# Kernel tuning notes

Hardware: AMD Instinct MI355X
Metric: run time of the kernel (lower is better)

## Reference

```python
import jax, jax.numpy as jnp
import numpy as np

EPS = 1e-5  # InstanceNorm2d default eps


def mesh_conv_point(x, neighbors, W, b):
    """MeshConvPoint: gather self+neighbor features, apply 1x(K+1) conv.
    x: [B, C, N]; neighbors: [B, N, K] int; W: [Cout, C, K+1]; b: [Cout]
    returns [B, Cout, N]
    """
    # gather neighbor features per batch: [B, C, N, K]
    g = jax.vmap(lambda xb, nb: xb[:, nb])(x, neighbors)
    G = jnp.concatenate([x[..., None], g], axis=-1)  # [B, C, N, K+1]
    return jnp.einsum('bcnk,ock->bon', G, W) + b[None, :, None]


def instance_norm(x):
    # InstanceNorm2d (affine=False) on [B, C, N, 1] == normalize over N per (b,c)
    mu = jnp.mean(x, axis=2, keepdims=True)
    var = jnp.var(x, axis=2, keepdims=True)
    return (x - mu) * jax.lax.rsqrt(var + EPS)


def setup_inputs() -> dict:
    key = jax.random.key(0)
    ks = jax.random.split(key, 10)
    B, Cin, Cout, N, K = 2, 256, 128, 30000, 6
    from_up = jax.random.normal(ks[0], (B, Cin, N), dtype=jnp.float32)
    from_down = jax.random.normal(ks[1], (B, Cout, N), dtype=jnp.float32)
    neighbors = jax.random.randint(ks[2], (B, N, K), 0, N)
    s = 0.05
    W_up = jax.random.normal(ks[3], (Cout, Cin, K + 1), dtype=jnp.float32) * s
    b_up = jnp.zeros((Cout,), dtype=jnp.float32)
    W_1 = jax.random.normal(ks[4], (Cout, 2 * Cout, K + 1), dtype=jnp.float32) * s
    b_1 = jnp.zeros((Cout,), dtype=jnp.float32)
    W_2 = jax.random.normal(ks[5], (Cout, Cout, K + 1), dtype=jnp.float32) * s
    b_2 = jnp.zeros((Cout,), dtype=jnp.float32)
    return {"from_up": from_up, "from_down": from_down, "neighbors": neighbors,
            "W_up": W_up, "b_up": b_up, "W_1": W_1, "b_1": b_1,
            "W_2": W_2, "b_2": b_2}


def reference(from_up, from_down, neighbors, W_up, b_up, W_1, b_1, W_2, b_2):
    # up_conv + squeeze(3)
    x1 = mesh_conv_point(from_up, neighbors, W_up, b_up)          # [B, Cout, N]
    # transfer_data: concat skip features along channels
    x1 = jnp.concatenate([x1, from_down], axis=1)                 # [B, 2*Cout, N]
    x1 = mesh_conv_point(x1, neighbors, W_1, b_1)                 # [B, Cout, N]
    x1 = instance_norm(x1)                                        # bn[0]
    # one conv2 block (blocks=1): conv + instance norm + residual
    x2 = mesh_conv_point(x1, neighbors, W_2, b_2)
    x2 = instance_norm(x2)                                        # bn[1]
    x2 = x2 + x1                                                  # residual
    return x2                                                     # [B, Cout, N]
```

## Files before the change

kernel.cpp:

```cpp
#include <hip/hip_runtime.h>

typedef __attribute__((ext_vector_type(8))) short short8;
typedef __attribute__((ext_vector_type(4))) float f32x4;

static __device__ __forceinline__ float bf2f(unsigned short u) {
    unsigned int x = ((unsigned int)u) << 16;
    union { unsigned int i; float f; } c; c.i = x; return c.f;
}
static __device__ __forceinline__ unsigned short f2bf(float f) {
    union { float f; unsigned int i; } c; c.f = f;
    unsigned int x = c.i;
    unsigned int r = (x + 0x7FFFu + ((x >> 16) & 1u)) >> 16;
    return (unsigned short)r;
}
static __device__ __forceinline__ void glds16(const char* g, char* l) {
    __builtin_amdgcn_global_load_lds(
        (const __attribute__((address_space(1))) unsigned int*)g,
        (__attribute__((address_space(3))) unsigned int*)l, 16, 0, 0);
}

__global__ void prepack_w2(const float* __restrict__ Wa, const float* __restrict__ Wb,
                           unsigned short* __restrict__ Wpa, unsigned short* __restrict__ Wpb,
                           int S) {
    int tid = blockIdx.x * blockDim.x + threadIdx.x;
    if (tid >= 2 * S * 512) return;
    const float* W = (tid < S * 512) ? Wa : Wb;
    unsigned short* Wp = (tid < S * 512) ? Wpa : Wpb;
    int rem = (tid < S * 512) ? tid : tid - S * 512;
    const int Cin = 256;
    int lane = rem & 63;
    int f = (rem >> 6) & 7;
    int s = rem >> 9;
    int o = f * 16 + (lane & 15);
    int kbase = s * 32 + 8 * (lane >> 4);
    unsigned short* dst = Wp + (size_t)rem * 8;
#pragma unroll
    for (int j = 0; j < 8; ++j) {
        int kk = kbase + j;
        int t = kk / Cin;
        int c = kk - t * Cin;
        dst[j] = f2bf(W[((size_t)o * Cin + c) * 7 + t]);
    }
}

__global__ void prepack_scaled_fold(const float* __restrict__ W, const float2* __restrict__ stats,
                                    unsigned short* __restrict__ Wp, const float* __restrict__ b2,
                                    float* __restrict__ b2out, int S, int nPre) {
    if ((int)blockIdx.x < nPre) {
        int tid = blockIdx.x * 256 + threadIdx.x;
        const int Cin = 128;
        int b = tid / (S * 512);
        int rem = tid - b * S * 512;
        int lane = rem & 63;
        int f = (rem >> 6) & 7;
        int s = rem >> 9;
        int o = f * 16 + (lane & 15);
        int kbase = s * 32 + 8 * (lane >> 4);
        unsigned short* dst = Wp + (size_t)tid * 8;
#pragma unroll
        for (int j = 0; j < 8; ++j) {
            int kk = kbase + j;
            int t = kk / Cin;
            int c = kk - t * Cin;
            float scale = stats[b * 128 + c].y;
            dst[j] = f2bf(W[((size_t)o * Cin + c) * 7 + t] * scale);
        }
    } else {
        int b = threadIdx.x >> 7, o = threadIdx.x & 127;
        float sum = 0.f;
        for (int c = 0; c < 128; ++c) {
            float2 st = stats[b * 128 + c];
            float sm = st.x * st.y;
            float ws = 0.f;
#pragma unroll
            for (int t = 0; t < 7; ++t) ws += W[((size_t)o * 128 + c) * 7 + t];
            sum += ws * sm;
        }
        b2out[b * 128 + o] = b2[o] - sum;
    }
}

__global__ void transpose_cast2(const float* __restrict__ up, const float* __restrict__ down,
                                unsigned short* __restrict__ upT, unsigned short* __restrict__ catT,
                                int N) {
    __shared__ __align__(16) unsigned short T[64 * 72];
    int b = blockIdx.z;
    int y = blockIdx.y;
    const float* in;  unsigned short* outp;  int c0, coff, C;
    if (y < 4) { in = up;   outp = upT;  c0 = y * 64;       coff = 0;   C = 256; }
    else       { in = down; outp = catT; c0 = (y - 4) * 64; coff = 128; C = 128; }
    int n0 = blockIdx.x * 64;
    const float* inb = in + (size_t)b * C * N;
    unsigned short* outb = outp + (size_t)b * N * 256;
    int tid = threadIdx.x;

    int nq = tid & 15, c_l = tid >> 4;
    bool nv = (n0 + nq * 4) < N;
    float4 v[4];
#pragma unroll
    for (int ci = 0; ci < 4; ++ci) {
        v[ci] = make_float4(0.f, 0.f, 0.f, 0.f);
        if (nv) v[ci] = *reinterpret_cast<const float4*>(
                            inb + (size_t)(c0 + ci * 16 + c_l) * N + n0 + nq * 4);
    }
#pragma unroll
    for (int ci = 0; ci < 4; ++ci) {
        int cl = ci * 16 + c_l;
        T[(nq * 4 + 0) * 72 + cl] = f2bf(v[ci].x);
        T[(nq * 4 + 1) * 72 + cl] = f2bf(v[ci].y);
        T[(nq * 4 + 2) * 72 + cl] = f2bf(v[ci].z);
        T[(nq * 4 + 3) * 72 + cl] = f2bf(v[ci].w);
    }
    __syncthreads();
    int c8 = tid & 7, n_l0 = tid >> 3;
#pragma unroll
    for (int p = 0; p < 2; ++p) {
        int n_l = p * 32 + n_l0;
        int n = n0 + n_l;
        if (n < N) {
            short8 u = *reinterpret_cast<const short8*>(&T[n_l * 72 + c8 * 8]);
            *reinterpret_cast<short8*>(&outb[(size_t)n * 256 + coff + c0 + c8 * 8]) = u;
        }
    }
}

template<int CS, int LD, bool STATS>
__global__ __launch_bounds__(512, 2) void conv_gemm(
    const unsigned short* __restrict__ src,
    const int* __restrict__ nbrs,
    const unsigned short* __restrict__ Wp, size_t w_bstride_bytes,
    const float* __restrict__ bias, int bias_bstride,
    unsigned short* __restrict__ dst,
    float2* __restrict__ part,
    int N, int coff)
{
    constexpr int ROWB = CS * 2;
    constexpr int SPT  = CS / 32;
    constexpr int S    = SPT * 7;
    constexpr int BUFB = 24576;

    const int tid  = threadIdx.x;
    const int lane = tid & 63;
    const int wid  = tid >> 6;
    const int pg   = wid & 3;
    const int h    = wid >> 2;
    const int l15  = lane & 15;
    const int ks   = lane >> 4;
    const int b    = blockIdx.y;
    const int pblk = blockIdx.x * 256;

    const char* srcb = (const char*)src + (size_t)b * N * ROWB;
    const char* wbc  = (const char*)Wp + (size_t)b * w_bstride_bytes;

    __shared__ char smem[4 * BUFB];

    int roffA[14];
    {
        int p = pblk + wid * 32 + (lane & 31);
        int pe = p < N ? p : N - 1;
        int offs[7];
        offs[0] = pe * ROWB;
        const int* nb = nbrs + ((size_t)b * N + pe) * 6;
#pragma unroll
        for (int t = 1; t < 7; ++t) offs[t] = nb[t - 1] * ROWB;
#pragma unroll
        for (int t = 0; t < 7; ++t)
#pragma unroll
            for (int i = 0; i < 2; ++i)
                roffA[t * 2 + i] = __shfl(offs[t], i * 16 + (lane >> 2));
    }
    asm volatile("s_waitcnt vmcnt(0)" ::: "memory");
    __builtin_amdgcn_sched_barrier(0);

    const int asw = (((lane & 3) ^ ((lane >> 2) & 3) ^ ((lane >> 4) & 3)) << 4);

    auto stage_all = [&](int t, int kk, int s, int buf) {
        char* base = smem + buf * BUFB;
#pragma unroll
        for (int i = 0; i < 2; ++i)
            glds16(srcb + roffA[t * 2 + i] + kk * 64 + asw,
                   base + (wid * 2 + i) * 1024);
        glds16(wbc + (size_t)s * 8192 + wid * 1024 + lane * 16,
               base + 16384 + wid * 1024);
    };

    f32x4 acc[4][4];
#pragma unroll
    for (int rg = 0; rg < 4; ++rg)
#pragma unroll
        for (int fi = 0; fi < 4; ++fi) acc[rg][fi] = (f32x4){0.f, 0.f, 0.f, 0.f};

    stage_all(0, 0, 0, 0);
    stage_all(1 / SPT, 1 % SPT, 1, 1);
    stage_all(2 / SPT, 2 % SPT, 2, 2);

    const int arsw = (((l15 & 3) ^ ((l15 >> 2) & 3)) << 4);

#pragma unroll
    for (int t = 0; t < 7; ++t) {
#pragma unroll
        for (int kk = 0; kk < SPT; ++kk) {
            const int s = t * SPT + kk;
            if (s + 2 < S)      { asm volatile("s_waitcnt vmcnt(6)" ::: "memory"); }
            else if (s + 1 < S) { asm volatile("s_waitcnt vmcnt(3)" ::: "memory"); }
            else                { asm volatile("s_waitcnt vmcnt(0)" ::: "memory"); }
            __builtin_amdgcn_sched_barrier(0);
            __builtin_amdgcn_s_barrier();
            __builtin_amdgcn_sched_barrier(0);
            if (s + 3 < S) {
                const int s3 = s + 3;
                stage_all(s3 / SPT, s3 % SPT, s3, s3 & 3);
            }

            const char* Ab = smem + (s & 3) * BUFB;
            const char* Wb = Ab + 16384;
            short8 a[4], w[4];
#pragma unroll
            for (int rg = 0; rg < 4; ++rg)
                a[rg] = *(const short8*)(Ab + (pg * 64 + rg * 16 + l15) * 64 +
                                         ((ks << 4) ^ arsw));
#pragma unroll
            for (int fi = 0; fi < 4; ++fi)
                w[fi] = *(const short8*)(Wb + (h * 4 + fi) * 1024 + lane * 16);
            __builtin_amdgcn_s_setprio(1);
#pragma unroll
            for (int rg = 0; rg < 4; ++rg)
#pragma unroll
                for (int fi = 0; fi < 4; ++fi)
                    acc[rg][fi] = __builtin_amdgcn_mfma_f32_16x16x32_bf16(
                        a[rg], w[fi], acc[rg][fi], 0, 0, 0);
            __builtin_amdgcn_s_setprio(0);
        }
    }

    const float* biasb = bias + (size_t)b * bias_bstride + h * 64;
    float bias_v[4];
#pragma unroll
    for (int fi = 0; fi < 4; ++fi) bias_v[fi] = biasb[fi * 16 + l15];

    unsigned short* dstb = dst + (size_t)b * N * LD + coff + h * 64;
#pragma unroll
    for (int rg = 0; rg < 4; ++rg) {
#pragma unroll
        for (int r = 0; r < 4; ++r) {
            int p = pblk + pg * 64 + rg * 16 + ks * 4 + r;
            if (p < N) {
#pragma unroll
                for (int fi = 0; fi < 4; ++fi)
                    dstb[(size_t)p * LD + fi * 16 + l15] = f2bf(acc[rg][fi][r] + bias_v[fi]);
            }
        }
    }

    if constexpr (STATS) {
        float s4[4], q4[4];
#pragma unroll
        for (int fi = 0; fi < 4; ++fi) { s4[fi] = 0.f; q4[fi] = 0.f; }
#pragma unroll
        for (int rg = 0; rg < 4; ++rg) {
#pragma unroll
            for (int r = 0; r < 4; ++r) {
                int p = pblk + pg * 64 + rg * 16 + ks * 4 + r;
                if (p < N) {
#pragma unroll
                    for (int fi = 0; fi < 4; ++fi) {
                        float v = acc[rg][fi][r] + bias_v[fi];
                        s4[fi] += v; q4[fi] += v * v;
                    }
                }
            }
        }
#pragma unroll
        for (int fi = 0; fi < 4; ++fi) {
            s4[fi] += __shfl_xor(s4[fi], 16); s4[fi] += __shfl_xor(s4[fi], 32);
            q4[fi] += __shfl_xor(q4[fi], 16); q4[fi] += __shfl_xor(q4[fi], 32);
        }
        __syncthreads();
        float* shs = (float*)smem;
        float* shq = shs + 512;
        if (lane < 16) {
#pragma unroll
            for (int fi = 0; fi < 4; ++fi) {
                shs[wid * 64 + fi * 16 + l15] = s4[fi];
                shq[wid * 64 + fi * 16 + l15] = q4[fi];
            }
        }
        __syncthreads();
        if (tid < 128) {
            int c = tid;
            int hh = c >> 6, cl = c & 63;
            float ss = 0.f, qq = 0.f;
#pragma unroll
            for (int p4 = 0; p4 < 4; ++p4) {
                ss += shs[(hh * 4 + p4) * 64 + cl];
                qq += shq[(hh * 4 + p4) * 64 + cl];
            }
            part[((size_t)b * gridDim.x + blockIdx.x) * 128 + c] = make_float2(ss, qq);
        }
    }
}

__global__ void stats_final(const float2* __restrict__ part, float2* __restrict__ stats,
                            int N, int NB) {
    int b = blockIdx.x;
    int c = threadIdx.x & 127;
    int r = threadIdx.x >> 7;
    float s = 0.f, sq = 0.f;
    const float2* p = part + (size_t)b * NB * 128 + c;
#pragma unroll 4
    for (int i = r; i < NB; i += 8) {
        float2 v = p[(size_t)i * 128];
        s += v.x; sq += v.y;
    }
    __shared__ float shs[8][128], shq[8][128];
    shs[r][c] = s; shq[r][c] = sq;
    __syncthreads();
    if (r == 0) {
#pragma unroll
        for (int i = 1; i < 8; ++i) { s += shs[i][c]; sq += shq[i][c]; }
        float mu = s / N;
        float var = sq / N - mu * mu;
        stats[b * 128 + c] = make_float2(mu, rsqrtf(var + 1e-5f));
    }
}

__global__ void final_k(const unsigned short* __restrict__ z, const unsigned short* __restrict__ x1,
                        const float2* __restrict__ stats1, const float2* __restrict__ stats2,
                        float* __restrict__ out, int N) {
    __shared__ float tile[32][133];
    int b = blockIdx.z;
    int n0 = blockIdx.x * 128, o0 = blockIdx.y * 32;
    int tid = threadIdx.x;
    const unsigned short* zb = z  + (size_t)b * N * 128;
    const unsigned short* xb = x1 + (size_t)b * N * 128;

    int oq = tid & 3, n_l0 = tid >> 2;
    float m1[8], r1[8], m2[8], r2[8];
#pragma unroll
    for (int j = 0; j < 8; ++j) {
        float2 s1 = stats1[b * 128 + o0 + oq * 8 + j];
        float2 s2 = stats2[b * 128 + o0 + oq * 8 + j];
        m1[j] = s1.x; r1[j] = s1.y; m2[j] = s2.x; r2[j] = s2.y;
    }
#pragma unroll
    for (int p = 0; p < 2; ++p) {
        int n_l = p * 64 + n_l0;
        int n = n0 + n_l;
        if (n < N) {
            short8 zv = *reinterpret_cast<const short8*>(zb + (size_t)n * 128 + o0 + oq * 8);
            short8 xv = *reinterpret_cast<const short8*>(xb + (size_t)n * 128 + o0 + oq * 8);
#pragma unroll
            for (int j = 0; j < 8; ++j) {
                float v = (bf2f((unsigned short)zv[j]) - m2[j]) * r2[j] +
                          (bf2f((unsigned short)xv[j]) - m1[j]) * r1[j];
                tile[oq * 8 + j][n_l] = v;
            }
        }
    }
    __syncthreads();
    float* ob = out + (size_t)b * 128 * N;
    int nq = tid & 31, o_l = tid >> 5;
    int n = n0 + nq * 4;
    if (n < N) {
#pragma unroll
        for (int pi = 0; pi < 4; ++pi) {
            int orow = pi * 8 + o_l;
            float4 v;
            v.x = tile[orow][nq * 4 + 0];
            v.y = tile[orow][nq * 4 + 1];
            v.z = tile[orow][nq * 4 + 2];
            v.w = tile[orow][nq * 4 + 3];
            *reinterpret_cast<float4*>(&ob[(size_t)(o0 + orow) * N + n]) = v;
        }
    }
}

extern "C" void kernel_launch(void* const* d_in, const int* in_sizes, int n_in,
                              void* d_out, int out_size, void* d_ws, size_t ws_size,
                              hipStream_t stream) {
    const float* from_up   = (const float*)d_in[0];
    const float* from_down = (const float*)d_in[1];
    const int*   neighbors = (const int*)d_in[2];
    const float* W_up = (const float*)d_in[3];
    const float* b_up = (const float*)d_in[4];
    const float* W_1  = (const float*)d_in[5];
    const float* b_1  = (const float*)d_in[6];
    const float* W_2  = (const float*)d_in[7];
    const float* b_2  = (const float*)d_in[8];
    float* out = (float*)d_out;

    const int B = 2, N = 30000;
    const int S1 = 56, S3 = 28;
    const int NBLK = (N + 255) / 256;

    char* ws = (char*)d_ws;
    size_t off = 0;
    auto alloc = [&](size_t bytes) {
        char* p = ws + off;
        off += (bytes + 255) & ~(size_t)255;
        return p;
    };
    unsigned short* upT   = (unsigned short*)alloc((size_t)B * N * 256 * 2);
    unsigned short* catT  = (unsigned short*)alloc((size_t)B * N * 256 * 2);
    unsigned short* x1    = (unsigned short*)alloc((size_t)B * N * 128 * 2);
    unsigned short* Wp0   = (unsigned short*)alloc((size_t)S1 * 512 * 8 * 2);
    unsigned short* Wp1   = (unsigned short*)alloc((size_t)S1 * 512 * 8 * 2);
    unsigned short* Wp2b  = (unsigned short*)alloc((size_t)B * S3 * 512 * 8 * 2);
    float*  b2fold = (float*)alloc((size_t)B * 128 * 4);
    float2* part   = (float2*)alloc((size_t)B * NBLK * 128 * 8);
    float2* stats1 = (float2*)alloc((size_t)B * 128 * 8);
    float2* stats2 = (float2*)alloc((size_t)B * 128 * 8);
    unsigned short* zbuf = upT;

    prepack_w2<<<(2 * S1 * 512 + 255) / 256, 256, 0, stream>>>(W_up, W_1, Wp0, Wp1, S1);

    transpose_cast2<<<dim3((N + 63) / 64, 6, B), 256, 0, stream>>>(from_up, from_down, upT, catT, N);

    dim3 cgrid(NBLK, B);
    conv_gemm<256, 256, false><<<cgrid, 512, 0, stream>>>(
        upT, neighbors, Wp0, 0, b_up, 0, catT, nullptr, N, 0);
    conv_gemm<256, 128, true><<<cgrid, 512, 0, stream>>>(
        catT, neighbors, Wp1, 0, b_1, 0, x1, part, N, 0);
    stats_final<<<B, 1024, 0, stream>>>((const float2*)part, stats1, N, NBLK);

    int nPre = (B * S3 * 512) / 256;
    prepack_scaled_fold<<<nPre + 1, 256, 0, stream>>>(W_2, stats1, Wp2b, b_2, b2fold, S3, nPre);

    conv_gemm<128, 128, true><<<cgrid, 512, 0, stream>>>(
        x1, neighbors, Wp2b, (size_t)S3 * 8192, b2fold, 128, zbuf, part, N, 0);
    stats_final<<<B, 1024, 0, stream>>>((const float2*)part, stats2, N, NBLK);

    final_k<<<dim3((N + 127) / 128, 4, B), 256, 0, stream>>>(zbuf, x1, stats1, stats2, out, N);
}
```

Baseline: 184.5 us.

## Fuse weight prepack into transpose kernel and process four n-tiles per block

Removes the separate prepack_w2 launch by handling weight packing in an extra grid row (y==6) of the transpose kernel. Each transpose block now covers 256 points in four 64-point stages. It double-buffers fp32 tiles in shared memory and prefetches the next stage's global loads into registers while converting the current one. This saves a launch and should overlap loads with conversion, but uses more shared memory per block and assigns the prepack to a small number of blocks.

```diff
diff --git a/kernel.cpp b/kernel.cpp
--- a/kernel.cpp
+++ b/kernel.cpp
@@ -17,30 +17,6 @@
     __builtin_amdgcn_global_load_lds(
         (const __attribute__((address_space(1))) unsigned int*)g,
         (__attribute__((address_space(3))) unsigned int*)l, 16, 0, 0);
-}
-
-__global__ void prepack_w2(const float* __restrict__ Wa, const float* __restrict__ Wb,
-                           unsigned short* __restrict__ Wpa, unsigned short* __restrict__ Wpb,
-                           int S) {
-    int tid = blockIdx.x * blockDim.x + threadIdx.x;
-    if (tid >= 2 * S * 512) return;
-    const float* W = (tid < S * 512) ? Wa : Wb;
-    unsigned short* Wp = (tid < S * 512) ? Wpa : Wpb;
-    int rem = (tid < S * 512) ? tid : tid - S * 512;
-    const int Cin = 256;
-    int lane = rem & 63;
-    int f = (rem >> 6) & 7;
-    int s = rem >> 9;
-    int o = f * 16 + (lane & 15);
-    int kbase = s * 32 + 8 * (lane >> 4);
-    unsigned short* dst = Wp + (size_t)rem * 8;
-#pragma unroll
-    for (int j = 0; j < 8; ++j) {
-        int kk = kbase + j;
-        int t = kk / Cin;
-        int c = kk - t * Cin;
-        dst[j] = f2bf(W[((size_t)o * Cin + c) * 7 + t]);
-    }
 }
 
 __global__ void prepack_scaled_fold(const float* __restrict__ W, const float2* __restrict__ stats,
@@ -82,45 +58,90 @@
 
 __global__ void transpose_cast2(const float* __restrict__ up, const float* __restrict__ down,
                                 unsigned short* __restrict__ upT, unsigned short* __restrict__ catT,
-                                int N) {
-    __shared__ __align__(16) unsigned short T[64 * 72];
+                                const float* __restrict__ W_up, const float* __restrict__ W_1,
+                                unsigned short* __restrict__ Wp0, unsigned short* __restrict__ Wp1,
+                                int S1, int N) {
+    int y = blockIdx.y;
+    if (y == 6) {
+        if (blockIdx.z != 0) return;
+        int units = 2 * S1 * 2;
+        for (int u = blockIdx.x; u < units; u += gridDim.x) {
+            int tid = u * 256 + threadIdx.x;
+            const float* W = (tid < S1 * 512) ? W_up : W_1;
+            unsigned short* Wp = (tid < S1 * 512) ? Wp0 : Wp1;
+            int rem = (tid < S1 * 512) ? tid : tid - S1 * 512;
+            const int Cin = 256;
+            int lane = rem & 63;
+            int f = (rem >> 6) & 7;
+            int s = rem >> 9;
+            int o = f * 16 + (lane & 15);
+            int kbase = s * 32 + 8 * (lane >> 4);
+            unsigned short* dst = Wp + (size_t)rem * 8;
+#pragma unroll
+            for (int j = 0; j < 8; ++j) {
+                int kk = kbase + j;
+                int t = kk / Cin;
+                int c = kk - t * Cin;
+                dst[j] = f2bf(W[((size_t)o * Cin + c) * 7 + t]);
+            }
+        }
+        return;
+    }
+
+    __shared__ float buf[2][64][65];
     int b = blockIdx.z;
-    int y = blockIdx.y;
     const float* in;  unsigned short* outp;  int c0, coff, C;
     if (y < 4) { in = up;   outp = upT;  c0 = y * 64;       coff = 0;   C = 256; }
     else       { in = down; outp = catT; c0 = (y - 4) * 64; coff = 128; C = 128; }
-    int n0 = blockIdx.x * 64;
+    int n_base = blockIdx.x * 256;
     const float* inb = in + (size_t)b * C * N;
     unsigned short* outb = outp + (size_t)b * N * 256;
     int tid = threadIdx.x;
 
     int nq = tid & 15, c_l = tid >> 4;
-    bool nv = (n0 + nq * 4) < N;
+    int c8 = tid & 7, n_l0 = tid >> 3;
+
     float4 v[4];
-#pragma unroll
-    for (int ci = 0; ci < 4; ++ci) {
-        v[ci] = make_float4(0.f, 0.f, 0.f, 0.f);
-        if (nv) v[ci] = *reinterpret_cast<const float4*>(
-                            inb + (size_t)(c0 + ci * 16 + c_l) * N + n0 + nq * 4);
-    }
-#pragma unroll
-    for (int ci = 0; ci < 4; ++ci) {
-        int cl = ci * 16 + c_l;
-        T[(nq * 4 + 0) * 72 + cl] = f2bf(v[ci].x);
-        T[(nq * 4 + 1) * 72 + cl] = f2bf(v[ci].y);
-        T[(nq * 4 + 2) * 72 + cl] = f2bf(v[ci].z);
-        T[(nq * 4 + 3) * 72 + cl] = f2bf(v[ci].w);
-    }
-    __syncthreads();
-    int c8 = tid & 7, n_l0 = tid >> 3;
-#pragma unroll
-    for (int p = 0; p < 2; ++p) {
-        int n_l = p * 32 + n_l0;
-        int n = n0 + n_l;
-        if (n < N) {
-            short8 u = *reinterpret_cast<const short8*>(&T[n_l * 72 + c8 * 8]);
-            *reinterpret_cast<short8*>(&outb[(size_t)n * 256 + coff + c0 + c8 * 8]) = u;
-        }
+    auto load_regs = [&](int st, float4 vv[4]) {
+        int n0s = n_base + st * 64;
+        bool nv = (n0s + nq * 4) < N;
+#pragma unroll
+        for (int ci = 0; ci < 4; ++ci) {
+            vv[ci] = make_float4(0.f, 0.f, 0.f, 0.f);
+            if (nv) vv[ci] = *reinterpret_cast<const float4*>(
+                                 inb + (size_t)(c0 + ci * 16 + c_l) * N + n0s + nq * 4);
+        }
+    };
+
+    load_regs(0, v);
+#pragma unroll
+    for (int st = 0; st < 4; ++st) {
+        float4 vn[4];
+        if (st < 3) load_regs(st + 1, vn);
+        float (*T)[65] = buf[st & 1];
+#pragma unroll
+        for (int ci = 0; ci < 4; ++ci) {
+            int cl = ci * 16 + c_l;
+            T[cl][nq * 4 + 0] = v[ci].x;
+            T[cl][nq * 4 + 1] = v[ci].y;
+            T[cl][nq * 4 + 2] = v[ci].z;
+            T[cl][nq * 4 + 3] = v[ci].w;
+        }
+        __syncthreads();
+        int n0s = n_base + st * 64;
+#pragma unroll
+        for (int p = 0; p < 2; ++p) {
+            int n_l = p * 32 + n_l0;
+            int n = n0s + n_l;
+            if (n < N) {
+                short8 u;
+#pragma unroll
+                for (int j = 0; j < 8; ++j) u[j] = (short)f2bf(T[c8 * 8 + j][n_l]);
+                *reinterpret_cast<short8*>(&outb[(size_t)n * 256 + coff + c0 + c8 * 8]) = u;
+            }
+        }
+#pragma unroll
+        for (int ci = 0; ci < 4; ++ci) v[ci] = vn[ci];
     }
 }
 
@@ -412,9 +433,8 @@
     float2* stats2 = (float2*)alloc((size_t)B * 128 * 8);
     unsigned short* zbuf = upT;
 
-    prepack_w2<<<(2 * S1 * 512 + 255) / 256, 256, 0, stream>>>(W_up, W_1, Wp0, Wp1, S1);
-
-    transpose_cast2<<<dim3((N + 63) / 64, 6, B), 256, 0, stream>>>(from_up, from_down, upT, catT, N);
+    transpose_cast2<<<dim3((N + 255) / 256, 7, B), 256, 0, stream>>>(
+        from_up, from_down, upT, catT, W_up, W_1, Wp0, Wp1, S1, N);
 
     dim3 cgrid(NBLK, B);
     conv_gemm<256, 256, false><<<cgrid, 512, 0, stream>>>(
```

New measurement: 176.6 us, median of 2. -4.3%, faster.
